# Kernel optimization log

Measured on AMD Instinct MI355X. Metric: run time of the kernel, lower is better.

The kernel has to match this reference:

```python
import jax, jax.numpy as jnp
import numpy as np
from jax.scipy.special import digamma

K_NEIGHBOURS = 5  # matches init_kwargs nNeighbours


def setup_inputs() -> dict:
    key = jax.random.key(0)
    k1, k2 = jax.random.split(key)
    x = jax.random.normal(k1, (2, 2, 64, 64), dtype=jnp.float32)
    y = jax.random.normal(k2, (2, 2, 64, 64), dtype=jnp.float32)
    return {"x": x, "y": y}


def _knn_mi(x, y, k):
    # KSG k-NN mutual information estimator, channel-wise.
    B, C, H, W = x.shape
    BC, HW = B * C, H * W
    xv = x.reshape(BC, HW)
    yv = y.reshape(BC, HW)
    # Pairwise L1 (scalar -> abs diff) distance matrices: (BC, HW, HW)
    dx = jnp.abs(xv[:, :, None] - xv[:, None, :])
    dy = jnp.abs(yv[:, :, None] - yv[:, None, :])
    # Joint-space Chebyshev distance (max over the two marginals)
    z = jnp.maximum(dx, dy)
    # eps = (k+1)-th smallest joint distance per point (includes self-distance 0),
    # matching torch .topk(k+1, largest=False).values[..., -1:]
    neg_smallest = jax.lax.top_k(-z, k + 1)[0]       # (BC, HW, k+1), descending in -z
    eps = -neg_smallest[:, :, -1:]                    # (BC, HW, 1)
    # Marginal neighbor counts with strict < eps (self included, as in torch code)
    nx = jnp.sum(dx < eps, axis=-1).astype(jnp.float32)  # (BC, HW)
    ny = jnp.sum(dy < eps, axis=-1).astype(jnp.float32)
    const = digamma(jnp.float32(k)) + digamma(jnp.float32(HW))
    mi = const - jnp.mean(digamma(nx) + digamma(ny), axis=-1)  # (BC,)
    return jnp.maximum(mi.reshape(B, C), 0.0)


def reference(x, y):
    return _knn_mi(x, y, K_NEIGHBOURS)
```

## Files before the change

### kernel.cpp

```cpp
#include <hip/hip_runtime.h>
#include <math.h>

#define HW 4096
#define NCH 4
#define TPB 256
#define G 16
#define ROWS_PER_BLOCK 16
#define BLOCKS_PER_CH (HW / ROWS_PER_BLOCK)
#define NBLOCKS (NCH * BLOCKS_PER_CH)
#define KNN 5

__device__ __forceinline__ float digammaf_dev(float x) {
    float r = 0.f;
    while (x < 6.f) { r -= 1.f / x; x += 1.f; }
    float f = 1.f / x, f2 = f * f;
    return logf(x) - 0.5f * f
         - f2 * (1.f / 12.f - f2 * (1.f / 120.f - f2 * (1.f / 252.f))) + r;
}

__device__ __forceinline__ void insert6(float (&s)[6], float d) {
    float n0 = fminf(s[0], d);
    float n1 = __builtin_amdgcn_fmed3f(s[0], s[1], d);
    float n2 = __builtin_amdgcn_fmed3f(s[1], s[2], d);
    float n3 = __builtin_amdgcn_fmed3f(s[2], s[3], d);
    float n4 = __builtin_amdgcn_fmed3f(s[3], s[4], d);
    float n5 = __builtin_amdgcn_fmed3f(s[4], s[5], d);
    s[0] = n0; s[1] = n1; s[2] = n2; s[3] = n3; s[4] = n4; s[5] = n5;
}

__global__ __launch_bounds__(TPB) void knnmi_rows(const float* __restrict__ x,
                                                  const float* __restrict__ y,
                                                  float* __restrict__ ws) {
    __shared__ float2 sxy[HW];
    __shared__ float red[ROWS_PER_BLOCK];

    const int c  = blockIdx.x >> 8;
    const int rb = blockIdx.x & 255;

    const float* xc = x + c * HW;
    const float* yc = y + c * HW;

    for (int i = threadIdx.x; i < HW / 4; i += TPB) {
        float4 xv = ((const float4*)xc)[i];
        float4 yv = ((const float4*)yc)[i];
        ((float4*)sxy)[2 * i]     = make_float4(xv.x, yv.x, xv.y, yv.y);
        ((float4*)sxy)[2 * i + 1] = make_float4(xv.z, yv.z, xv.w, yv.w);
    }
    __syncthreads();

    const int wv   = threadIdx.x >> 6;
    const int lane = threadIdx.x & 63;
    const int l    = lane & (G - 1);
    const int g    = lane >> 4;
    const int row  = rb * ROWS_PER_BLOCK + wv * 4 + g;

    const float2 pr = sxy[row];
    const float xi = pr.x, yi = pr.y;

    const float4* f4 = (const float4*)sxy;

    float s[6];
#pragma unroll
    for (int q = 0; q < 6; ++q) s[q] = 3.4e38f;

#pragma unroll 8
    for (int it = 0; it < HW / (2 * G); ++it) {
        float4 p = f4[it * G + l];
        float d0 = fmaxf(fabsf(xi - p.x), fabsf(yi - p.y));
        float d1 = fmaxf(fabsf(xi - p.z), fabsf(yi - p.w));
        insert6(s, d0);
        insert6(s, d1);
    }

#pragma unroll
    for (int m = 1; m < G; m <<= 1) {
        float o[6];
#pragma unroll
        for (int q = 0; q < 6; ++q) o[q] = __shfl_xor(s[q], m);
#pragma unroll
        for (int q = 0; q < 6; ++q) insert6(s, o[q]);
    }
    const float eps = s[5];

    int nx = 0, ny = 0;
#pragma unroll 8
    for (int it = 0; it < HW / (2 * G); ++it) {
        float4 p = f4[it * G + l];
        nx += (fabsf(xi - p.x) < eps);
        ny += (fabsf(yi - p.y) < eps);
        nx += (fabsf(xi - p.z) < eps);
        ny += (fabsf(yi - p.w) < eps);
    }

    int pk = (nx << 16) | ny;
#pragma unroll
    for (int m = 1; m < G; m <<= 1) pk += __shfl_xor(pk, m);

    if (l == 0)
        red[wv * 4 + g] = digammaf_dev((float)(pk >> 16))
                        + digammaf_dev((float)(pk & 0xffff));
    __syncthreads();

    if (threadIdx.x == 0) {
        float v = 0.f;
#pragma unroll
        for (int q = 0; q < ROWS_PER_BLOCK; ++q) v += red[q];
        ws[blockIdx.x] = v;
    }
}

__global__ void knnmi_final(const float* __restrict__ ws, float* __restrict__ out) {
    const int w    = threadIdx.x >> 6;
    const int lane = threadIdx.x & 63;
    float sum = 0.f;
#pragma unroll
    for (int i = lane; i < BLOCKS_PER_CH; i += 64) sum += ws[w * BLOCKS_PER_CH + i];
#pragma unroll
    for (int m = 32; m; m >>= 1) sum += __shfl_xor(sum, m);
    if (lane == 0) {
        float mi = digammaf_dev((float)KNN) + digammaf_dev((float)HW)
                 - sum / (float)HW;
        out[w] = fmaxf(mi, 0.f);
    }
}

extern "C" void kernel_launch(void* const* d_in, const int* in_sizes, int n_in,
                              void* d_out, int out_size, void* d_ws, size_t ws_size,
                              hipStream_t stream) {
    const float* x = (const float*)d_in[0];
    const float* y = (const float*)d_in[1];
    float* out = (float*)d_out;
    float* ws  = (float*)d_ws;

    knnmi_rows<<<NBLOCKS, TPB, 0, stream>>>(x, y, ws);
    knnmi_final<<<1, NCH * 64, 0, stream>>>(ws, out);
}
```

Baseline: 35.29 us.

## Bucket points by value and search kNN and counts only in nearby bins

Adds a bucketizing kernel that sorts each channel's points into 512 fixed-width bins by x (and separately by y) and stores prefix offsets in workspace. The row kernel then grows a window outward from the point's x-bin until the 6th-smallest Chebyshev distance is bounded by the bin edges. It computes marginal counts from prefix sums plus exact checks only in the boundary bins. This replaces the O(HW^2) brute-force scans with near-local searches. The cost is an extra serial single-block-per-channel kernel launch, a fixed value range for the bins, and divergent variable-length loops.

```diff
diff --git a/kernel.cpp b/kernel.cpp
--- a/kernel.cpp
+++ b/kernel.cpp
@@ -4,11 +4,27 @@
 #define HW 4096
 #define NCH 4
 #define TPB 256
-#define G 16
 #define ROWS_PER_BLOCK 16
 #define BLOCKS_PER_CH (HW / ROWS_PER_BLOCK)
 #define NBLOCKS (NCH * BLOCKS_PER_CH)
 #define KNN 5
+
+#define NBINS 512
+#define BLO   (-5.0f)
+#define BINV  51.2f
+#define BDELTA 0.01953125f
+#define SLOP  1e-5f
+#define INFT  3.4e38f
+
+#define WS_BXY   16384
+#define WS_BY    32768
+#define WS_PREF  49152
+#define WS_PART  57344
+
+__device__ __forceinline__ int binOf(float v) {
+    int b = (int)floorf((v - BLO) * BINV);
+    return min(max(b, 0), NBINS - 1);
+}
 
 __device__ __forceinline__ float digammaf_dev(float x) {
     float r = 0.f;
@@ -28,52 +44,143 @@
     s[0] = n0; s[1] = n1; s[2] = n2; s[3] = n3; s[4] = n4; s[5] = n5;
 }
 
-__global__ __launch_bounds__(TPB) void knnmi_rows(const float* __restrict__ x,
-                                                  const float* __restrict__ y,
-                                                  float* __restrict__ ws) {
+__global__ __launch_bounds__(TPB) void knnmi_bucketize(const float* __restrict__ x,
+                                                       const float* __restrict__ y,
+                                                       float* __restrict__ ws) {
+    __shared__ int h[NBINS], tmp[NBINS], cur[NBINS];
+    const int c = blockIdx.x;
+    const int t = threadIdx.x;
+    const float* xc = x + c * HW;
+    const float* yc = y + c * HW;
+    float* bxx = ws + c * HW;
+    float* bxy = ws + WS_BXY + c * HW;
+    float* by  = ws + WS_BY  + c * HW;
+    int* prefx = (int*)ws + WS_PREF + c * (NBINS + 1);
+    int* prefy = (int*)ws + WS_PREF + NCH * (NBINS + 1) + c * (NBINS + 1);
+
+    for (int i = t; i < NBINS; i += TPB) h[i] = 0;
+    __syncthreads();
+    for (int i = t; i < HW; i += TPB) atomicAdd(&h[binOf(xc[i])], 1);
+    __syncthreads();
+    for (int off = 1; off < NBINS; off <<= 1) {
+        for (int i = t; i < NBINS; i += TPB)
+            tmp[i] = h[i] + ((i >= off) ? h[i - off] : 0);
+        __syncthreads();
+        for (int i = t; i < NBINS; i += TPB) h[i] = tmp[i];
+        __syncthreads();
+    }
+    for (int i = t; i < NBINS; i += TPB) {
+        int e = (i == 0) ? 0 : h[i - 1];
+        prefx[i] = e;
+        cur[i] = e;
+    }
+    if (t == 0) prefx[NBINS] = h[NBINS - 1];
+    __syncthreads();
+    for (int i = t; i < HW; i += TPB) {
+        float xv = xc[i], yv = yc[i];
+        int pos = atomicAdd(&cur[binOf(xv)], 1);
+        bxx[pos] = xv;
+        bxy[pos] = yv;
+    }
+    __syncthreads();
+
+    for (int i = t; i < NBINS; i += TPB) h[i] = 0;
+    __syncthreads();
+    for (int i = t; i < HW; i += TPB) atomicAdd(&h[binOf(yc[i])], 1);
+    __syncthreads();
+    for (int off = 1; off < NBINS; off <<= 1) {
+        for (int i = t; i < NBINS; i += TPB)
+            tmp[i] = h[i] + ((i >= off) ? h[i - off] : 0);
+        __syncthreads();
+        for (int i = t; i < NBINS; i += TPB) h[i] = tmp[i];
+        __syncthreads();
+    }
+    for (int i = t; i < NBINS; i += TPB) {
+        int e = (i == 0) ? 0 : h[i - 1];
+        prefy[i] = e;
+        cur[i] = e;
+    }
+    if (t == 0) prefy[NBINS] = h[NBINS - 1];
+    __syncthreads();
+    for (int i = t; i < HW; i += TPB) {
+        float yv = yc[i];
+        int pos = atomicAdd(&cur[binOf(yv)], 1);
+        by[pos] = yv;
+    }
+}
+
+__global__ __launch_bounds__(TPB, 4) void knnmi_rows(float* __restrict__ ws) {
     __shared__ float2 sxy[HW];
+    __shared__ int pfx[NBINS + 1];
     __shared__ float red[ROWS_PER_BLOCK];
 
     const int c  = blockIdx.x >> 8;
     const int rb = blockIdx.x & 255;
-
-    const float* xc = x + c * HW;
-    const float* yc = y + c * HW;
+    const float* bxx = ws + c * HW;
+    const float* bxy = ws + WS_BXY + c * HW;
+    const float* by  = ws + WS_BY  + c * HW;
+    const int* prefx = (const int*)ws + WS_PREF + c * (NBINS + 1);
+    const int* prefy = (const int*)ws + WS_PREF + NCH * (NBINS + 1) + c * (NBINS + 1);
+    float* partials  = ws + WS_PART;
 
     for (int i = threadIdx.x; i < HW / 4; i += TPB) {
-        float4 xv = ((const float4*)xc)[i];
-        float4 yv = ((const float4*)yc)[i];
+        float4 xv = ((const float4*)bxx)[i];
+        float4 yv = ((const float4*)bxy)[i];
         ((float4*)sxy)[2 * i]     = make_float4(xv.x, yv.x, xv.y, yv.y);
         ((float4*)sxy)[2 * i + 1] = make_float4(xv.z, yv.z, xv.w, yv.w);
     }
+    for (int i = threadIdx.x; i <= NBINS; i += TPB) pfx[i] = prefx[i];
     __syncthreads();
 
     const int wv   = threadIdx.x >> 6;
     const int lane = threadIdx.x & 63;
-    const int l    = lane & (G - 1);
+    const int l    = lane & 15;
     const int g    = lane >> 4;
-    const int row  = rb * ROWS_PER_BLOCK + wv * 4 + g;
-
-    const float2 pr = sxy[row];
-    const float xi = pr.x, yi = pr.y;
-
-    const float4* f4 = (const float4*)sxy;
+    const int p    = rb * ROWS_PER_BLOCK + wv * 4 + g;
+
+    const float xi = sxy[p].x;
+    const float yi = sxy[p].y;
+    const int myB  = binOf(xi);
 
     float s[6];
 #pragma unroll
-    for (int q = 0; q < 6; ++q) s[q] = 3.4e38f;
-
-#pragma unroll 8
-    for (int it = 0; it < HW / (2 * G); ++it) {
-        float4 p = f4[it * G + l];
-        float d0 = fmaxf(fabsf(xi - p.x), fabsf(yi - p.y));
-        float d1 = fmaxf(fabsf(xi - p.z), fabsf(yi - p.w));
-        insert6(s, d0);
-        insert6(s, d1);
-    }
-
-#pragma unroll
-    for (int m = 1; m < G; m <<= 1) {
+    for (int q = 0; q < 6; ++q) s[q] = INFT;
+
+    const int oLo = pfx[myB], oHi = pfx[myB + 1];
+    for (int tt = oLo + l; tt < oHi; tt += 16) {
+        float2 pp = sxy[tt];
+        insert6(s, fmaxf(fabsf(xi - pp.x), fabsf(yi - pp.y)));
+    }
+
+    int idxL = oLo, idxR = oHi;
+    for (int w = 0; w < 300; ++w) {
+        int newL = max(idxL - 16, 0);
+        int newR = min(idxR + 16, HW);
+        int tL = newL + l;
+        int tR = idxR + l;
+        float2 pL = sxy[tL];
+        float2 pR = sxy[min(tR, HW - 1)];
+        float dL = (tL < idxL) ? fmaxf(fabsf(xi - pL.x), fabsf(yi - pL.y)) : INFT;
+        float dR = (tR < newR) ? fmaxf(fabsf(xi - pR.x), fabsf(yi - pR.y)) : INFT;
+        insert6(s, dL);
+        insert6(s, dR);
+        idxL = newL; idxR = newR;
+
+        float edgeL = (idxL == 0) ? INFT
+            : (xi - (BLO + (float)(binOf(sxy[max(idxL - 1, 0)].x) + 1) * BDELTA + SLOP));
+        float edgeR = (idxR >= HW) ? INFT
+            : ((BLO + (float)binOf(sxy[min(idxR, HW - 1)].x) * BDELTA - SLOP) - xi);
+
+        unsigned long long mL = __ballot(s[5] <= edgeL);
+        unsigned long long mR = __ballot(s[5] <= edgeR);
+        int gb = lane & 48;
+        bool conv = (((mL >> gb) & 0xFFFFull) != 0ull) &&
+                    (((mR >> gb) & 0xFFFFull) != 0ull);
+        if (__all(conv)) break;
+    }
+
+#pragma unroll
+    for (int m = 1; m < 16; m <<= 1) {
         float o[6];
 #pragma unroll
         for (int q = 0; q < 6; ++q) o[q] = __shfl_xor(s[q], m);
@@ -82,19 +189,41 @@
     }
     const float eps = s[5];
 
-    int nx = 0, ny = 0;
-#pragma unroll 8
-    for (int it = 0; it < HW / (2 * G); ++it) {
-        float4 p = f4[it * G + l];
-        nx += (fabsf(xi - p.x) < eps);
-        ny += (fabsf(yi - p.y) < eps);
-        nx += (fabsf(xi - p.z) < eps);
-        ny += (fabsf(yi - p.w) < eps);
+    int nx = 0;
+    {
+        int loB = binOf(xi - eps), hiB = binOf(xi + eps);
+        int fLo = loB + 2, fHi = hiB - 2;
+        if (fLo <= fHi) {
+            if (l == 0) nx += pfx[fHi + 1] - pfx[fLo];
+            int a0 = pfx[max(loB - 1, 0)], a1 = pfx[min(loB + 1, NBINS - 1) + 1];
+            int b0 = pfx[max(hiB - 1, 0)], b1 = pfx[min(hiB + 1, NBINS - 1) + 1];
+            for (int tt = a0 + l; tt < a1; tt += 16) nx += (fabsf(sxy[tt].x - xi) < eps);
+            for (int tt = b0 + l; tt < b1; tt += 16) nx += (fabsf(sxy[tt].x - xi) < eps);
+        } else {
+            int a0 = pfx[max(loB - 1, 0)], a1 = pfx[min(hiB + 1, NBINS - 1) + 1];
+            for (int tt = a0 + l; tt < a1; tt += 16) nx += (fabsf(sxy[tt].x - xi) < eps);
+        }
+    }
+
+    int ny = 0;
+    {
+        int loB = binOf(yi - eps), hiB = binOf(yi + eps);
+        int fLo = loB + 2, fHi = hiB - 2;
+        if (fLo <= fHi) {
+            if (l == 0) ny += prefy[fHi + 1] - prefy[fLo];
+            int a0 = prefy[max(loB - 1, 0)], a1 = prefy[min(loB + 1, NBINS - 1) + 1];
+            int b0 = prefy[max(hiB - 1, 0)], b1 = prefy[min(hiB + 1, NBINS - 1) + 1];
+            for (int tt = a0 + l; tt < a1; tt += 16) ny += (fabsf(by[tt] - yi) < eps);
+            for (int tt = b0 + l; tt < b1; tt += 16) ny += (fabsf(by[tt] - yi) < eps);
+        } else {
+            int a0 = prefy[max(loB - 1, 0)], a1 = prefy[min(hiB + 1, NBINS - 1) + 1];
+            for (int tt = a0 + l; tt < a1; tt += 16) ny += (fabsf(by[tt] - yi) < eps);
+        }
     }
 
     int pk = (nx << 16) | ny;
 #pragma unroll
-    for (int m = 1; m < G; m <<= 1) pk += __shfl_xor(pk, m);
+    for (int m = 1; m < 16; m <<= 1) pk += __shfl_xor(pk, m);
 
     if (l == 0)
         red[wv * 4 + g] = digammaf_dev((float)(pk >> 16))
@@ -105,16 +234,18 @@
         float v = 0.f;
 #pragma unroll
         for (int q = 0; q < ROWS_PER_BLOCK; ++q) v += red[q];
-        ws[blockIdx.x] = v;
+        partials[blockIdx.x] = v;
     }
 }
 
 __global__ void knnmi_final(const float* __restrict__ ws, float* __restrict__ out) {
+    const float* partials = ws + WS_PART;
     const int w    = threadIdx.x >> 6;
     const int lane = threadIdx.x & 63;
     float sum = 0.f;
 #pragma unroll
-    for (int i = lane; i < BLOCKS_PER_CH; i += 64) sum += ws[w * BLOCKS_PER_CH + i];
+    for (int i = lane; i < BLOCKS_PER_CH; i += 64)
+        sum += partials[w * BLOCKS_PER_CH + i];
 #pragma unroll
     for (int m = 32; m; m >>= 1) sum += __shfl_xor(sum, m);
     if (lane == 0) {
@@ -132,6 +263,7 @@
     float* out = (float*)d_out;
     float* ws  = (float*)d_ws;
 
-    knnmi_rows<<<NBLOCKS, TPB, 0, stream>>>(x, y, ws);
+    knnmi_bucketize<<<NCH, TPB, 0, stream>>>(x, y, ws);
+    knnmi_rows<<<NBLOCKS, TPB, 0, stream>>>(ws);
     knnmi_final<<<1, NCH * 64, 0, stream>>>(ws, out);
 }
```

Result: slower. 71.47 us (+102.5%).
